# Kernel tuning notes

Measured on AMD Instinct MI355X. Metric: run time of the kernel, lower is better.

## Reference

```python
import jax, jax.numpy as jnp
import numpy as np

LN_EPS = 1e-5


def setup_inputs() -> dict:
    key = jax.random.key(0)
    ks = jax.random.split(key, 6)
    B, N, C, H = 8, 4096, 768, 12
    D = C // H
    x = jax.random.normal(ks[0], (B, N, C), dtype=jnp.float32)
    w_qkv = jax.random.normal(ks[1], (3 * C, C), dtype=jnp.float32) * (C ** -0.5)
    w_proj = jax.random.normal(ks[2], (C, C), dtype=jnp.float32) * (C ** -0.5)
    b_proj = jnp.zeros((C,), dtype=jnp.float32)
    # trunc_normal_(std=0.02) approximated by clipped normal
    p1 = jnp.clip(jax.random.normal(ks[3], (H, N), dtype=jnp.float32) * 0.02, -0.04, 0.04)
    p2 = jnp.clip(jax.random.normal(ks[4], (H, N), dtype=jnp.float32) * 0.02, -0.04, 0.04)
    gamma = jnp.ones((D,), dtype=jnp.float32)
    beta = jnp.zeros((D,), dtype=jnp.float32)
    return {"x": x, "w_qkv": w_qkv, "w_proj": w_proj, "b_proj": b_proj,
            "p1": p1, "p2": p2, "gamma": gamma, "beta": beta}


def _layernorm(h, gamma, beta):
    mu = jnp.mean(h, axis=-1, keepdims=True)
    var = jnp.var(h, axis=-1, keepdims=True)
    return (h - mu) * jax.lax.rsqrt(var + LN_EPS) * gamma + beta


def reference(x, w_qkv, w_proj, b_proj, p1, p2, gamma, beta):
    B, N, C = x.shape
    H = p1.shape[0]
    D = C // H
    # qkv projection (no bias): [B,N,3C] -> [3,B,H,N,D]
    qkv = (x @ w_qkv.T).reshape(B, N, 3, H, D).transpose(2, 0, 3, 1, 4)
    q, k, v = qkv[0], qkv[1], qkv[2]
    # weighted k*v reduction over sequence: [B,H,D]
    modulator = jnp.einsum('hn,bhnd->bhd', p2, k * v)
    modulator = _layernorm(modulator, gamma, beta)
    # broadcast modulation back over N: [B,H,N,D]
    modulator = jnp.einsum('hn,bhd->bhnd', p1, modulator)
    out = (q * modulator).transpose(0, 2, 1, 3).reshape(B, N, C)
    return out @ w_proj.T + b_proj
```

## Files before the change

### kernel.cpp

```cpp
#include <hip/hip_runtime.h>
#include <stdint.h>
#include <stddef.h>

#define LN_EPS 1e-5f

typedef __bf16 bf16;
typedef __bf16 bf16x8 __attribute__((ext_vector_type(8)));
typedef __bf16 bf16x4 __attribute__((ext_vector_type(4)));
typedef float f32x4 __attribute__((ext_vector_type(4)));

#define GL16(gp, lp)                                                                   \
  __builtin_amdgcn_global_load_lds((__attribute__((address_space(1))) uint32_t*)(gp),  \
                                   (__attribute__((address_space(3))) uint32_t*)(lp),  \
                                   16, 0, 0)

__global__ __launch_bounds__(256) void cvt_kernel(const float* __restrict__ src,
                                                  bf16* __restrict__ dst, int n4) {
  int i = blockIdx.x * 256 + threadIdx.x;
  if (i >= n4) return;
  const float4 v = ((const float4*)src)[i];
  bf16x4 o;
  o[0] = (bf16)v.x; o[1] = (bf16)v.y; o[2] = (bf16)v.z; o[3] = (bf16)v.w;
  ((bf16x4*)dst)[i] = o;
}

__device__ __forceinline__ void gemm_core_768(const bf16* __restrict__ At,
                                              const bf16* __restrict__ Bt,
                                              bf16* lA, bf16* lB,
                                              f32x4 acc[4][4]) {
  const int tid  = threadIdx.x;
  const int wave = tid >> 6;
  const int lane = tid & 63;
  const int l16  = lane & 15;

  const int srow = wave * 32 + (lane >> 2);
  const int gq   = (lane & 3) ^ ((lane >> 3) & 3);
  const int scol = gq * 8;
  const bf16* gA0 = At + srow * 768 + scol;
  const bf16* gA1 = gA0 + 16 * 768;
  const bf16* gB0 = Bt + srow * 768 + scol;
  const bf16* gB1 = gB0 + 16 * 768;
  bf16* sA0 = lA + wave * 1024 + lane * 8;
  bf16* sA1 = sA0 + 512;
  bf16* sB0 = lB + wave * 1024 + lane * 8;
  bf16* sB1 = sB0 + 512;

  const int wm = (wave & 1) * 64;
  const int wn = (wave >> 1) * 64;
  const int qg = lane >> 4;
  const int sw = (l16 >> 1) & 3;
  const int rdoff = ((qg ^ sw) * 8);

  for (int kt = 0; kt < 768; kt += 32) {
    GL16(gA0 + kt, sA0);
    GL16(gA1 + kt, sA1);
    GL16(gB0 + kt, sB0);
    GL16(gB1 + kt, sB1);
    __syncthreads();

    bf16x8 aF[4], bF[4];
#pragma unroll
    for (int i = 0; i < 4; i++)
      aF[i] = *(const bf16x8*)(lA + (wm + i * 16 + l16) * 32 + rdoff);
#pragma unroll
    for (int j = 0; j < 4; j++)
      bF[j] = *(const bf16x8*)(lB + (wn + j * 16 + l16) * 32 + rdoff);

#pragma unroll
    for (int i = 0; i < 4; i++)
#pragma unroll
      for (int j = 0; j < 4; j++)
        acc[i][j] = __builtin_amdgcn_mfma_f32_16x16x32_bf16(aF[i], bF[j], acc[i][j], 0, 0, 0);

    __syncthreads();
  }
}

__global__ __launch_bounds__(256) void gemm_qkv(const bf16* __restrict__ A,
                                                const bf16* __restrict__ B,
                                                bf16* __restrict__ C) {
  __shared__ __align__(16) bf16 lA[128 * 32];
  __shared__ __align__(16) bf16 lB[128 * 32];
  f32x4 acc[4][4] = {};

  const int m0 = blockIdx.x * 128;
  const int n0 = blockIdx.y * 128;
  gemm_core_768(A + (size_t)m0 * 768, B + (size_t)n0 * 768, lA, lB, acc);

  const int tid = threadIdx.x, wave = tid >> 6, lane = tid & 63;
  const int row0 = m0 + (wave & 1) * 64 + (lane >> 4) * 4;
  const int col0 = n0 + (wave >> 1) * 64 + (lane & 15);
#pragma unroll
  for (int i = 0; i < 4; i++)
#pragma unroll
    for (int j = 0; j < 4; j++)
#pragma unroll
      for (int r = 0; r < 4; r++)
        C[(size_t)(row0 + i * 16 + r) * 2304 + col0 + j * 16] = (bf16)acc[i][j][r];
}

__global__ __launch_bounds__(192) void mod_partial(const bf16* __restrict__ qkv,
                                                   const float* __restrict__ p2,
                                                   float* __restrict__ partials) {
  const int chunk = blockIdx.x, b = blockIdx.y;
  const int t = threadIdx.x;
  const int c  = t % 96;
  const int rp = t / 96;
  const int h  = c >> 3;
  const int n0 = chunk * 64;

  const bf16* kp  = qkv + ((size_t)(b * 4096 + n0 + rp)) * 2304 + 768 + c * 8;
  const float* pw = p2 + h * 4096 + n0 + rp;

  float acc[8] = {0.f, 0.f, 0.f, 0.f, 0.f, 0.f, 0.f, 0.f};
#pragma unroll 4
  for (int i = 0; i < 32; i++) {
    const bf16* kpi = kp + (size_t)i * 2 * 2304;
    const bf16x8 kv = *(const bf16x8*)(kpi);
    const bf16x8 vv = *(const bf16x8*)(kpi + 768);
    const float p = pw[2 * i];
#pragma unroll
    for (int j = 0; j < 8; j++)
      acc[j] += p * (float)kv[j] * (float)vv[j];
  }

  __shared__ float red[2][96][8];
#pragma unroll
  for (int j = 0; j < 8; j++) red[rp][c][j] = acc[j];
  __syncthreads();
  if (t < 96) {
    float* o = partials + ((size_t)(b * 64 + chunk)) * 768 + c * 8;
#pragma unroll
    for (int j = 0; j < 8; j++) o[j] = red[0][c][j] + red[1][c][j];
  }
}

__global__ __launch_bounds__(64) void mod_reduce_ln(const float* __restrict__ partials,
                                                    const float* __restrict__ gamma,
                                                    const float* __restrict__ beta,
                                                    float* __restrict__ mod) {
  const int h = blockIdx.x, b = blockIdx.y;
  const int d = threadIdx.x;

  const float* p = partials + (size_t)(b * 64) * 768 + h * 64 + d;
  float s = 0.f;
#pragma unroll 8
  for (int chunk = 0; chunk < 64; chunk++) s += p[(size_t)chunk * 768];

  float sum = s, sumsq = s * s;
#pragma unroll
  for (int o = 32; o > 0; o >>= 1) {
    sum   += __shfl_xor(sum, o);
    sumsq += __shfl_xor(sumsq, o);
  }
  const float mu  = sum * (1.f / 64.f);
  const float var = sumsq * (1.f / 64.f) - mu * mu;
  const float r   = rsqrtf(var + LN_EPS);
  mod[(b * 12 + h) * 64 + d] = (s - mu) * r * gamma[d] + beta[d];
}

__global__ __launch_bounds__(256) void modulate(const bf16* __restrict__ qkv,
                                                const float* __restrict__ p1,
                                                const float* __restrict__ mod,
                                                bf16* __restrict__ amod) {
  const int v = blockIdx.x * 256 + threadIdx.x;
  if (v >= 32768 * 96) return;
  const int m  = v / 96;
  const int cv = v - m * 96;
  const int c0 = cv * 8;
  const int b  = m >> 12;
  const int n  = m & 4095;
  const int h  = c0 >> 6;

  const bf16x8 q = *(const bf16x8*)(qkv + (size_t)m * 2304 + c0);
  const float pv = p1[h * 4096 + n];
  const float4 m0 = *(const float4*)(mod + b * 768 + c0);
  const float4 m1 = *(const float4*)(mod + b * 768 + c0 + 4);

  bf16x8 o;
  o[0] = (bf16)((float)q[0] * pv * m0.x);
  o[1] = (bf16)((float)q[1] * pv * m0.y);
  o[2] = (bf16)((float)q[2] * pv * m0.z);
  o[3] = (bf16)((float)q[3] * pv * m0.w);
  o[4] = (bf16)((float)q[4] * pv * m1.x);
  o[5] = (bf16)((float)q[5] * pv * m1.y);
  o[6] = (bf16)((float)q[6] * pv * m1.z);
  o[7] = (bf16)((float)q[7] * pv * m1.w);
  *(bf16x8*)(amod + (size_t)m * 768 + c0) = o;
}

__global__ __launch_bounds__(256) void gemm_proj(const bf16* __restrict__ A,
                                                 const bf16* __restrict__ B,
                                                 const float* __restrict__ bias,
                                                 float* __restrict__ C) {
  __shared__ __align__(16) bf16 lA[128 * 32];
  __shared__ __align__(16) bf16 lB[128 * 32];
  f32x4 acc[4][4] = {};

  const int m0 = blockIdx.x * 128;
  const int n0 = blockIdx.y * 128;
  gemm_core_768(A + (size_t)m0 * 768, B + (size_t)n0 * 768, lA, lB, acc);

  const int tid = threadIdx.x, wave = tid >> 6, lane = tid & 63;
  const int row0 = m0 + (wave & 1) * 64 + (lane >> 4) * 4;
  const int col0 = n0 + (wave >> 1) * 64 + (lane & 15);
#pragma unroll
  for (int j = 0; j < 4; j++) {
    const int col = col0 + j * 16;
    const float bv = bias[col];
#pragma unroll
    for (int i = 0; i < 4; i++)
#pragma unroll
      for (int r = 0; r < 4; r++)
        C[(size_t)(row0 + i * 16 + r) * 768 + col] = acc[i][j][r] + bv;
  }
}

extern "C" void kernel_launch(void* const* d_in, const int* in_sizes, int n_in,
                              void* d_out, int out_size, void* d_ws, size_t ws_size,
                              hipStream_t stream) {
  (void)in_sizes; (void)n_in; (void)out_size; (void)ws_size;

  const float* x      = (const float*)d_in[0];
  const float* w_qkv  = (const float*)d_in[1];
  const float* w_proj = (const float*)d_in[2];
  const float* b_proj = (const float*)d_in[3];
  const float* p1     = (const float*)d_in[4];
  const float* p2     = (const float*)d_in[5];
  const float* gamma  = (const float*)d_in[6];
  const float* beta   = (const float*)d_in[7];
  float* out = (float*)d_out;

  char* ws = (char*)d_ws;
  bf16*  xb   = (bf16*)(ws + 0);
  bf16*  wqb  = (bf16*)(ws + 50331648);
  bf16*  wpb  = (bf16*)(ws + 53870592);
  bf16*  qkv  = (bf16*)(ws + 55050240);
  float* mod  = (float*)(ws + 206045184);
  float* partials = (float*)(ws + 0);
  bf16*  amod     = (bf16*)(ws + 0);

  cvt_kernel<<<24576, 256, 0, stream>>>(x, xb, 6291456);
  cvt_kernel<<<1728,  256, 0, stream>>>(w_qkv, wqb, 442368);
  cvt_kernel<<<576,   256, 0, stream>>>(w_proj, wpb, 147456);

  gemm_qkv<<<dim3(256, 18), 256, 0, stream>>>(xb, wqb, qkv);

  mod_partial<<<dim3(64, 8), 192, 0, stream>>>(qkv, p2, partials);
  mod_reduce_ln<<<dim3(12, 8), 64, 0, stream>>>(partials, gamma, beta, mod);

  modulate<<<12288, 256, 0, stream>>>(qkv, p1, mod, amod);

  gemm_proj<<<dim3(256, 6), 256, 0, stream>>>(amod, wpb, b_proj, out);
}
```

Baseline: 436.2 us.

## Fuse K/V reduction and Q modulation into GEMM epilogues, drop QKV buffer

Removes the full 2304-wide QKV intermediate. A K/V GEMM kernel per head and row block writes K and V tiles to shared memory and reduces p2*k*v directly into per-block partials. The Q GEMM applies the p1*mod scaling in its epilogue and writes amod. The three conversion launches are merged into one, and the grid order is swapped so consecutive blocks share A rows. This saves heavy global traffic and separate launches, at the cost of K/V GEMM tiles of only 64 columns each and an extra LDS pass.

```diff
diff --git a/kernel.cpp b/kernel.cpp
--- a/kernel.cpp
+++ b/kernel.cpp
@@ -14,18 +14,27 @@
                                    (__attribute__((address_space(3))) uint32_t*)(lp),  \
                                    16, 0, 0)
 
-__global__ __launch_bounds__(256) void cvt_kernel(const float* __restrict__ src,
-                                                  bf16* __restrict__ dst, int n4) {
+#define XV4   6291456
+#define WQV4  442368
+#define WPV4  147456
+__global__ __launch_bounds__(256) void cvt_all(const float* __restrict__ x,
+                                               const float* __restrict__ wq,
+                                               const float* __restrict__ wp,
+                                               bf16* __restrict__ xb,
+                                               bf16* __restrict__ wqb,
+                                               bf16* __restrict__ wpb) {
   int i = blockIdx.x * 256 + threadIdx.x;
-  if (i >= n4) return;
-  const float4 v = ((const float4*)src)[i];
+  const float* src; bf16* dst; int off;
+  if (i < XV4)              { src = x;  dst = xb;  off = i; }
+  else if (i < XV4 + WQV4)  { src = wq; dst = wqb; off = i - XV4; }
+  else                      { src = wp; dst = wpb; off = i - (XV4 + WQV4); }
+  const float4 v = ((const float4*)src)[off];
   bf16x4 o;
   o[0] = (bf16)v.x; o[1] = (bf16)v.y; o[2] = (bf16)v.z; o[3] = (bf16)v.w;
-  ((bf16x4*)dst)[i] = o;
-}
-
-__device__ __forceinline__ void gemm_core_768(const bf16* __restrict__ At,
-                                              const bf16* __restrict__ Bt,
+  ((bf16x4*)dst)[off] = o;
+}
+
+__device__ __forceinline__ void gemm_core_768(const bf16* At, const bf16* Bt,
                                               bf16* lA, bf16* lB,
                                               f32x4 acc[4][4]) {
   const int tid  = threadIdx.x;
@@ -76,62 +85,53 @@
   }
 }
 
-__global__ __launch_bounds__(256) void gemm_qkv(const bf16* __restrict__ A,
-                                                const bf16* __restrict__ B,
-                                                bf16* __restrict__ C) {
-  __shared__ __align__(16) bf16 lA[128 * 32];
-  __shared__ __align__(16) bf16 lB[128 * 32];
+__global__ __launch_bounds__(256) void kv_gemm_reduce(const bf16* __restrict__ A,
+                                                      const bf16* __restrict__ B,
+                                                      const float* __restrict__ p2,
+                                                      float* __restrict__ partials) {
+  __shared__ __align__(16) bf16 sKV[2 * 128 * 68];
+  __shared__ float red[4][64];
+  bf16* lA = sKV;
+  bf16* lB = sKV + 4096;
+
+  const int h    = blockIdx.x;
+  const int mblk = blockIdx.y;
+  const int m0   = mblk * 128;
+  const int tid  = threadIdx.x, wave = tid >> 6, lane = tid & 63;
+
+  const bf16* Bt = B + (size_t)(wave < 2 ? (768 + h * 64) : (1536 + h * 64 - 64)) * 768;
+
   f32x4 acc[4][4] = {};
-
-  const int m0 = blockIdx.x * 128;
-  const int n0 = blockIdx.y * 128;
-  gemm_core_768(A + (size_t)m0 * 768, B + (size_t)n0 * 768, lA, lB, acc);
-
-  const int tid = threadIdx.x, wave = tid >> 6, lane = tid & 63;
-  const int row0 = m0 + (wave & 1) * 64 + (lane >> 4) * 4;
-  const int col0 = n0 + (wave >> 1) * 64 + (lane & 15);
+  gemm_core_768(A + (size_t)m0 * 768, Bt, lA, lB, acc);
+
+  const int kv    = wave >> 1;
+  const int row_l = (wave & 1) * 64 + (lane >> 4) * 4;
+  const int d_l   = lane & 15;
+  bf16* sT = sKV + kv * (128 * 68);
 #pragma unroll
   for (int i = 0; i < 4; i++)
 #pragma unroll
     for (int j = 0; j < 4; j++)
 #pragma unroll
       for (int r = 0; r < 4; r++)
-        C[(size_t)(row0 + i * 16 + r) * 2304 + col0 + j * 16] = (bf16)acc[i][j][r];
-}
-
-__global__ __launch_bounds__(192) void mod_partial(const bf16* __restrict__ qkv,
-                                                   const float* __restrict__ p2,
-                                                   float* __restrict__ partials) {
-  const int chunk = blockIdx.x, b = blockIdx.y;
-  const int t = threadIdx.x;
-  const int c  = t % 96;
-  const int rp = t / 96;
-  const int h  = c >> 3;
-  const int n0 = chunk * 64;
-
-  const bf16* kp  = qkv + ((size_t)(b * 4096 + n0 + rp)) * 2304 + 768 + c * 8;
-  const float* pw = p2 + h * 4096 + n0 + rp;
-
-  float acc[8] = {0.f, 0.f, 0.f, 0.f, 0.f, 0.f, 0.f, 0.f};
-#pragma unroll 4
-  for (int i = 0; i < 32; i++) {
-    const bf16* kpi = kp + (size_t)i * 2 * 2304;
-    const bf16x8 kv = *(const bf16x8*)(kpi);
-    const bf16x8 vv = *(const bf16x8*)(kpi + 768);
-    const float p = pw[2 * i];
-#pragma unroll
-    for (int j = 0; j < 8; j++)
-      acc[j] += p * (float)kv[j] * (float)vv[j];
-  }
-
-  __shared__ float red[2][96][8];
-#pragma unroll
-  for (int j = 0; j < 8; j++) red[rp][c][j] = acc[j];
+        sT[(row_l + i * 16 + r) * 68 + j * 16 + d_l] = (bf16)acc[i][j][r];
   __syncthreads();
-  if (t < 96) {
-    float* o = partials + ((size_t)(b * 64 + chunk)) * 768 + c * 8;
-#pragma unroll
-    for (int j = 0; j < 8; j++) o[j] = red[0][c][j] + red[1][c][j];
+
+  const int d  = tid & 63;
+  const int ch = tid >> 6;
+  const int n_base = (m0 & 4095) + ch * 32;
+  const float* pw = p2 + h * 4096 + n_base;
+  const bf16* sk = sKV + (ch * 32) * 68 + d;
+  const bf16* sv = sk + 128 * 68;
+  float s = 0.f;
+#pragma unroll 8
+  for (int n = 0; n < 32; n++)
+    s += pw[n] * (float)sk[n * 68] * (float)sv[n * 68];
+  red[ch][d] = s;
+  __syncthreads();
+  if (tid < 64) {
+    partials[((size_t)mblk * 12 + h) * 64 + tid] =
+        red[0][tid] + red[1][tid] + red[2][tid] + red[3][tid];
   }
 }
 
@@ -142,10 +142,10 @@
   const int h = blockIdx.x, b = blockIdx.y;
   const int d = threadIdx.x;
 
-  const float* p = partials + (size_t)(b * 64) * 768 + h * 64 + d;
+  const float* p = partials + ((size_t)(b * 32) * 12 + h) * 64 + d;
   float s = 0.f;
 #pragma unroll 8
-  for (int chunk = 0; chunk < 64; chunk++) s += p[(size_t)chunk * 768];
+  for (int mb = 0; mb < 32; mb++) s += p[(size_t)mb * 12 * 64];
 
   float sum = s, sumsq = s * s;
 #pragma unroll
@@ -159,34 +159,43 @@
   mod[(b * 12 + h) * 64 + d] = (s - mu) * r * gamma[d] + beta[d];
 }
 
-__global__ __launch_bounds__(256) void modulate(const bf16* __restrict__ qkv,
-                                                const float* __restrict__ p1,
-                                                const float* __restrict__ mod,
-                                                bf16* __restrict__ amod) {
-  const int v = blockIdx.x * 256 + threadIdx.x;
-  if (v >= 32768 * 96) return;
-  const int m  = v / 96;
-  const int cv = v - m * 96;
-  const int c0 = cv * 8;
-  const int b  = m >> 12;
-  const int n  = m & 4095;
-  const int h  = c0 >> 6;
-
-  const bf16x8 q = *(const bf16x8*)(qkv + (size_t)m * 2304 + c0);
-  const float pv = p1[h * 4096 + n];
-  const float4 m0 = *(const float4*)(mod + b * 768 + c0);
-  const float4 m1 = *(const float4*)(mod + b * 768 + c0 + 4);
-
-  bf16x8 o;
-  o[0] = (bf16)((float)q[0] * pv * m0.x);
-  o[1] = (bf16)((float)q[1] * pv * m0.y);
-  o[2] = (bf16)((float)q[2] * pv * m0.z);
-  o[3] = (bf16)((float)q[3] * pv * m0.w);
-  o[4] = (bf16)((float)q[4] * pv * m1.x);
-  o[5] = (bf16)((float)q[5] * pv * m1.y);
-  o[6] = (bf16)((float)q[6] * pv * m1.z);
-  o[7] = (bf16)((float)q[7] * pv * m1.w);
-  *(bf16x8*)(amod + (size_t)m * 768 + c0) = o;
+__global__ __launch_bounds__(256) void q_gemm_mod(const bf16* __restrict__ A,
+                                                  const bf16* __restrict__ B,
+                                                  const float* __restrict__ p1,
+                                                  const float* __restrict__ mod,
+                                                  bf16* __restrict__ amod) {
+  __shared__ __align__(16) bf16 lA[128 * 32];
+  __shared__ __align__(16) bf16 lB[128 * 32];
+  f32x4 acc[4][4] = {};
+
+  const int n0 = blockIdx.x * 128;
+  const int m0 = blockIdx.y * 128;
+  gemm_core_768(A + (size_t)m0 * 768, B + (size_t)n0 * 768, lA, lB, acc);
+
+  const int tid = threadIdx.x, wave = tid >> 6, lane = tid & 63;
+  const int row0 = m0 + (wave & 1) * 64 + (lane >> 4) * 4;
+  const int col0 = n0 + (wave >> 1) * 64 + (lane & 15);
+  const int b    = m0 >> 12;
+  const int h    = (n0 + (wave >> 1) * 64) >> 6;
+
+  float p1v[4][4];
+#pragma unroll
+  for (int i = 0; i < 4; i++)
+#pragma unroll
+    for (int r = 0; r < 4; r++)
+      p1v[i][r] = p1[h * 4096 + ((row0 + i * 16 + r) & 4095)];
+  float mv[4];
+#pragma unroll
+  for (int j = 0; j < 4; j++) mv[j] = mod[b * 768 + col0 + j * 16];
+
+#pragma unroll
+  for (int i = 0; i < 4; i++)
+#pragma unroll
+    for (int j = 0; j < 4; j++)
+#pragma unroll
+      for (int r = 0; r < 4; r++)
+        amod[(size_t)(row0 + i * 16 + r) * 768 + col0 + j * 16] =
+            (bf16)(acc[i][j][r] * p1v[i][r] * mv[j]);
 }
 
 __global__ __launch_bounds__(256) void gemm_proj(const bf16* __restrict__ A,
@@ -197,8 +206,8 @@
   __shared__ __align__(16) bf16 lB[128 * 32];
   f32x4 acc[4][4] = {};
 
-  const int m0 = blockIdx.x * 128;
-  const int n0 = blockIdx.y * 128;
+  const int n0 = blockIdx.x * 128;
+  const int m0 = blockIdx.y * 128;
   gemm_core_768(A + (size_t)m0 * 768, B + (size_t)n0 * 768, lA, lB, acc);
 
   const int tid = threadIdx.x, wave = tid >> 6, lane = tid & 63;
@@ -232,24 +241,20 @@
   float* out = (float*)d_out;
 
   char* ws = (char*)d_ws;
-  bf16*  xb   = (bf16*)(ws + 0);
-  bf16*  wqb  = (bf16*)(ws + 50331648);
-  bf16*  wpb  = (bf16*)(ws + 53870592);
-  bf16*  qkv  = (bf16*)(ws + 55050240);
-  float* mod  = (float*)(ws + 206045184);
-  float* partials = (float*)(ws + 0);
-  bf16*  amod     = (bf16*)(ws + 0);
-
-  cvt_kernel<<<24576, 256, 0, stream>>>(x, xb, 6291456);
-  cvt_kernel<<<1728,  256, 0, stream>>>(w_qkv, wqb, 442368);
-  cvt_kernel<<<576,   256, 0, stream>>>(w_proj, wpb, 147456);
-
-  gemm_qkv<<<dim3(256, 18), 256, 0, stream>>>(xb, wqb, qkv);
-
-  mod_partial<<<dim3(64, 8), 192, 0, stream>>>(qkv, p2, partials);
+  bf16*  xb       = (bf16*)(ws + 0);
+  bf16*  wqb      = (bf16*)(ws + 50331648);
+  bf16*  wpb      = (bf16*)(ws + 53870592);
+  bf16*  amod     = (bf16*)(ws + 55050240);
+  float* partials = (float*)(ws + 105381888);
+  float* mod      = (float*)(ws + 106168320);
+
+  cvt_all<<<26880, 256, 0, stream>>>(x, w_qkv, w_proj, xb, wqb, wpb);
+
+  kv_gemm_reduce<<<dim3(12, 256), 256, 0, stream>>>(xb, wqb, p2, partials);
+
   mod_reduce_ln<<<dim3(12, 8), 64, 0, stream>>>(partials, gamma, beta, mod);
 
-  modulate<<<12288, 256, 0, stream>>>(qkv, p1, mod, amod);
-
-  gemm_proj<<<dim3(256, 6), 256, 0, stream>>>(amod, wpb, b_proj, out);
-}
+  q_gemm_mod<<<dim3(6, 256), 256, 0, stream>>>(xb, wqb, p1, mod, amod);
+
+  gemm_proj<<<dim3(6, 256), 256, 0, stream>>>(amod, wpb, b_proj, out);
+}
```

Measured after the change: 408.4 us. 6.4% less time.
